# Optimization experiments

Measured on AMD Instinct MI355X. Metric: run time of the kernel, lower is better.

Reference implementation:

```python
import jax, jax.numpy as jnp
import numpy as np


def setup_inputs() -> dict:
    key = jax.random.key(0)
    ks = jax.random.split(key, 9)
    B, S, D, DK, DV = 4, 4096, 1024, 128, 128
    scale = 1.0 / np.sqrt(D)
    return {
        "q": jax.random.normal(ks[0], (B, S, D), jnp.float32),
        "k": jax.random.normal(ks[1], (B, S, D), jnp.float32),
        "v": jax.random.normal(ks[2], (B, S, D), jnp.float32),
        "Wq": jax.random.normal(ks[3], (D, DK), jnp.float32) * scale,
        "bq": jnp.zeros((DK,), jnp.float32),
        "Wk": jax.random.normal(ks[4], (D, DK), jnp.float32) * scale,
        "bk": jnp.zeros((DK,), jnp.float32),
        "Wv": jax.random.normal(ks[5], (D, DV), jnp.float32) * scale,
        "bv": jnp.zeros((DV,), jnp.float32),
    }


def reference(q, k, v, Wq, bq, Wk, bk, Wv, bv):
    # Q/K/V projections (nn.Linear)
    Q = q @ Wq + bq          # [B,S,DK]
    K = k @ Wk + bk          # [B,S,DK]
    V = v @ Wv + bv          # [B,S,DV]
    scale = Q.shape[-1] ** 0.5
    scores = jnp.einsum("bqd,bkd->bqk", Q, K) / scale  # [B,Sq,Sk]
    attn = jax.nn.softmax(scores, axis=-1)
    return jnp.einsum("bqk,bkd->bqd", attn, V)          # [B,Sq,DV]
```

## Files before the change

### kernel.cpp

```cpp
#include <hip/hip_runtime.h>
#include <hip/hip_bf16.h>
#include <cstdint>
#include <cmath>


typedef __bf16 bf16x8 __attribute__((ext_vector_type(8)));
typedef float f32x4 __attribute__((ext_vector_type(4)));
typedef float f32x16 __attribute__((ext_vector_type(16)));

__device__ __forceinline__ unsigned short f2bf(float f) {
  unsigned u = __float_as_uint(f);
  u += 0x7fffu + ((u >> 16) & 1u);
  return (unsigned short)(u >> 16);
}

__device__ __forceinline__ bf16x8 ld_frag(const char* p) {
  uint4 u = *reinterpret_cast<const uint4*>(p);
  return __builtin_bit_cast(bf16x8, u);
}

__device__ __forceinline__ unsigned cvtpk_bf16(float lo, float hi) {
  unsigned r;
  asm("v_cvt_pk_bf16_f32 %0, %1, %2" : "=v"(r) : "v"(lo), "v"(hi));
  return r;
}

__device__ __forceinline__ void pl32swap(unsigned &a, unsigned &b) {
  asm("v_permlane32_swap_b32 %0, %1" : "+v"(a), "+v"(b));
}

__device__ __forceinline__ bf16x8 mk_frag(unsigned w0, unsigned w1, unsigned w2, unsigned w3) {
  uint4 u{w0, w1, w2, w3};
  return __builtin_bit_cast(bf16x8, u);
}

#define QSCALE_LOG2E 0.12751744f

__global__ __launch_bounds__(256) void prep_wt_kernel(const float* __restrict__ W,
                                                      unsigned short* __restrict__ Wt) {
  __shared__ float tile[64][65];
  int kt = blockIdx.x, nt = blockIdx.y;
  int tid = threadIdx.x;
  int c = tid & 63;
  int r0 = (tid >> 6) * 16;
#pragma unroll
  for (int i = 0; i < 16; ++i) {
    int r = r0 + i;
    tile[r][c] = W[(size_t)(kt * 64 + r) * 128 + nt * 64 + c];
  }
  __syncthreads();
#pragma unroll
  for (int i = 0; i < 16; ++i) {
    int n = r0 + i;
    Wt[(size_t)(nt * 64 + n) * 1024 + kt * 64 + c] = f2bf(tile[c][n]);
  }
}

__global__ __launch_bounds__(256) void proj_kernel(
    const float* __restrict__ qx, const float* __restrict__ kx, const float* __restrict__ vx,
    const unsigned short* __restrict__ Wtq, const unsigned short* __restrict__ Wtk,
    const unsigned short* __restrict__ Wtv,
    const float* __restrict__ bq, const float* __restrict__ bk, const float* __restrict__ bv,
    unsigned short* __restrict__ Qb, unsigned short* __restrict__ Kb,
    unsigned short* __restrict__ Vtb) {
  const int mode = blockIdx.y;
  const float* x = (mode == 0) ? qx : (mode == 1) ? kx : vx;
  const unsigned short* Wt = (mode == 0) ? Wtq : (mode == 1) ? Wtk : Wtv;
  const float* bias = (mode == 0) ? bq : (mode == 1) ? bk : bv;

  __shared__ uint4 ldsA4[1024];
  __shared__ uint4 ldsW4[1024];
  char* ldsA = (char*)ldsA4;
  char* ldsW = (char*)ldsW4;

  const int tid = threadIdx.x;
  const int lane = tid & 63, wid = tid >> 6;
  const int l15 = lane & 15, hi = lane >> 4;
  const int wm = wid >> 1, wn = wid & 1;
  const long row0 = (long)blockIdx.x * 128;

  f32x4 acc[4][4];
#pragma unroll
  for (int i = 0; i < 4; ++i)
#pragma unroll
    for (int j = 0; j < 4; ++j) acc[i][j] = f32x4{0.f, 0.f, 0.f, 0.f};

  for (int kt = 0; kt < 16; ++kt) {
    const int k0 = kt * 64;
#pragma unroll
    for (int i = 0; i < 4; ++i) {
      int u = tid + 256 * i;
      int row = u >> 3, c8 = u & 7;
      const float* src = x + (row0 + row) * 1024 + k0 + c8 * 8;
      float4 f0 = *reinterpret_cast<const float4*>(src);
      float4 f1 = *reinterpret_cast<const float4*>(src + 4);
      uint4 w;
      w.x = (unsigned)f2bf(f0.x) | ((unsigned)f2bf(f0.y) << 16);
      w.y = (unsigned)f2bf(f0.z) | ((unsigned)f2bf(f0.w) << 16);
      w.z = (unsigned)f2bf(f1.x) | ((unsigned)f2bf(f1.y) << 16);
      w.w = (unsigned)f2bf(f1.z) | ((unsigned)f2bf(f1.w) << 16);
      int off = (row * 128 + c8 * 16) ^ ((row & 7) << 4);
      *reinterpret_cast<uint4*>(ldsA + off) = w;
      const unsigned short* wsrc = Wt + (size_t)row * 1024 + k0 + c8 * 8;
      uint4 wv = *reinterpret_cast<const uint4*>(wsrc);
      *reinterpret_cast<uint4*>(ldsW + off) = wv;
    }
    __syncthreads();
#pragma unroll
    for (int kk = 0; kk < 2; ++kk) {
      bf16x8 af[4], bfv[4];
#pragma unroll
      for (int mi = 0; mi < 4; ++mi) {
        int row = wm * 64 + mi * 16 + l15;
        af[mi] = ld_frag(ldsA + ((row * 128 + kk * 64 + hi * 16) ^ ((row & 7) << 4)));
      }
#pragma unroll
      for (int ni = 0; ni < 4; ++ni) {
        int row = wn * 64 + ni * 16 + l15;
        bfv[ni] = ld_frag(ldsW + ((row * 128 + kk * 64 + hi * 16) ^ ((row & 7) << 4)));
      }
#pragma unroll
      for (int mi = 0; mi < 4; ++mi)
#pragma unroll
        for (int ni = 0; ni < 4; ++ni)
          acc[mi][ni] = __builtin_amdgcn_mfma_f32_16x16x32_bf16(af[mi], bfv[ni], acc[mi][ni], 0, 0, 0);
    }
    __syncthreads();
  }

#pragma unroll
  for (int ni = 0; ni < 4; ++ni) {
    int n = wn * 64 + ni * 16 + l15;
    float bv_ = bias[n];
#pragma unroll
    for (int mi = 0; mi < 4; ++mi) {
      long m = row0 + wm * 64 + mi * 16 + hi * 4;
      f32x4 a = acc[mi][ni];
      if (mode == 2) {
        int bb = (int)(m >> 12);
        int s = (int)(m & 4095);
        ushort4 pk;
        pk.x = f2bf(a.x + bv_); pk.y = f2bf(a.y + bv_);
        pk.z = f2bf(a.z + bv_); pk.w = f2bf(a.w + bv_);
        *reinterpret_cast<ushort4*>(Vtb + ((size_t)(bb * 128 + n)) * 4096 + s) = pk;
      } else {
        const float sc = (mode == 0) ? QSCALE_LOG2E : 1.0f;
        unsigned short* outp = (mode == 0) ? Qb : Kb;
        outp[(m + 0) * 128 + n] = f2bf((a.x + bv_) * sc);
        outp[(m + 1) * 128 + n] = f2bf((a.y + bv_) * sc);
        outp[(m + 2) * 128 + n] = f2bf((a.z + bv_) * sc);
        outp[(m + 3) * 128 + n] = f2bf((a.w + bv_) * sc);
      }
    }
  }
}

__global__ __launch_bounds__(256, 2) void attn_kernel(
    const unsigned short* __restrict__ Qb, const unsigned short* __restrict__ Kb,
    const unsigned short* __restrict__ Vtb, float* __restrict__ Po,
    float* __restrict__ ml, int tps) {
  __shared__ uint4 ldsK4[1024];
  __shared__ uint4 ldsV4[1024];
  char* ldsK = (char*)ldsK4;
  char* ldsV = (char*)ldsV4;

  const int tid = threadIdx.x;
  const int lane = tid & 63, wid = tid >> 6;
  const int l31 = lane & 31, hi = lane >> 5;
  const int split = blockIdx.y;
  const int b = blockIdx.z;
  const int qbase = blockIdx.x * 128 + wid * 32;
  const size_t growq = (size_t)b * 4096 + qbase + l31;

  bf16x8 qf[8];
  {
    const unsigned short* qp = Qb + growq * 128 + hi * 8;
#pragma unroll
    for (int kt = 0; kt < 8; ++kt)
      qf[kt] = __builtin_bit_cast(bf16x8, *reinterpret_cast<const uint4*>(qp + kt * 16));
  }

  f32x16 oacc[4];
#pragma unroll
  for (int d = 0; d < 4; ++d)
#pragma unroll
    for (int j = 0; j < 16; ++j) oacc[d][j] = 0.f;
  float mrun = -INFINITY, lrun = 0.f;

  const int t0 = split * tps, t1 = t0 + tps;

  for (int t = t0; t < t1; ++t) {
    const int kv0 = t * 64;
    const char* kg = (const char*)Kb + ((size_t)(b * 4096) + kv0) * 256;
#pragma unroll
    for (int i = 0; i < 4; ++i) {
      int u = tid + 256 * i;
      int row = u >> 4, c = u & 15;
      uint4 val = *reinterpret_cast<const uint4*>(kg + row * 256 + c * 16);
      *reinterpret_cast<uint4*>(ldsK + ((row * 256 + c * 16) ^ ((row & 7) << 4))) = val;
    }
    const char* vg = (const char*)Vtb + (size_t)b * 128 * 4096 * 2 + (size_t)kv0 * 2;
#pragma unroll
    for (int i = 0; i < 4; ++i) {
      int u = tid + 256 * i;
      int dv = u >> 3, c = u & 7;
      uint4 val = *reinterpret_cast<const uint4*>(vg + (size_t)dv * 8192 + c * 16);
      *reinterpret_cast<uint4*>(ldsV + ((dv * 128 + c * 16) ^ ((dv & 7) << 4))) = val;
    }
    __syncthreads();

    f32x16 sc0, sc1;
#pragma unroll
    for (int j = 0; j < 16; ++j) { sc0[j] = 0.f; sc1[j] = 0.f; }
    __builtin_amdgcn_s_setprio(1);
#pragma unroll
    for (int kvb = 0; kvb < 2; ++kvb) {
      int row = kvb * 32 + l31;
      int rowoff = row * 256, swz = (row & 7) << 4;
#pragma unroll
      for (int kt = 0; kt < 8; ++kt) {
        bf16x8 kf = ld_frag(ldsK + ((rowoff + kt * 32 + hi * 16) ^ swz));
        if (kvb == 0) sc0 = __builtin_amdgcn_mfma_f32_32x32x16_bf16(kf, qf[kt], sc0, 0, 0, 0);
        else          sc1 = __builtin_amdgcn_mfma_f32_32x32x16_bf16(kf, qf[kt], sc1, 0, 0, 0);
      }
    }
    __builtin_amdgcn_s_setprio(0);

    float tmx[16];
#pragma unroll
    for (int i = 0; i < 16; ++i) tmx[i] = fmaxf(sc0[i], sc1[i]);
#pragma unroll
    for (int s = 8; s > 0; s >>= 1)
#pragma unroll
      for (int i = 0; i < s; ++i) tmx[i] = fmaxf(tmx[i], tmx[i + s]);
    float mt = tmx[0];
    mt = fmaxf(mt, __shfl_xor(mt, 32));

    if (!__all(mt - mrun <= 8.0f)) {
      float mnew = fmaxf(mrun, mt);
      float scl = exp2f(mrun - mnew);
      mrun = mnew;
      lrun *= scl;
#pragma unroll
      for (int d = 0; d < 4; ++d)
#pragma unroll
        for (int j = 0; j < 16; ++j) oacc[d][j] *= scl;
    }

#pragma unroll
    for (int i = 0; i < 16; ++i) {
      sc0[i] = exp2f(sc0[i] - mrun);
      sc1[i] = exp2f(sc1[i] - mrun);
    }
    float ts[16];
#pragma unroll
    for (int i = 0; i < 16; ++i) ts[i] = sc0[i] + sc1[i];
#pragma unroll
    for (int s = 8; s > 0; s >>= 1)
#pragma unroll
      for (int i = 0; i < s; ++i) ts[i] += ts[i + s];
    float psum = ts[0];
    psum += __shfl_xor(psum, 32);
    lrun += psum;

    bf16x8 pa[4];
#pragma unroll
    for (int c = 0; c < 2; ++c) {
      const f32x16& p = c ? sc1 : sc0;
#pragma unroll
      for (int g = 0; g < 2; ++g) {
        const int base = g * 8;
        unsigned a0 = cvtpk_bf16(p[base + 0], p[base + 1]);
        unsigned b0 = cvtpk_bf16(p[base + 4], p[base + 5]);
        pl32swap(a0, b0);
        unsigned a1 = cvtpk_bf16(p[base + 2], p[base + 3]);
        unsigned b1 = cvtpk_bf16(p[base + 6], p[base + 7]);
        pl32swap(a1, b1);
        pa[c * 2 + g] = mk_frag(a0, a1, b0, b1);
      }
    }

    __builtin_amdgcn_s_setprio(1);
#pragma unroll
    for (int dvb = 0; dvb < 4; ++dvb) {
      int vrow = dvb * 32 + l31;
      int voff = vrow * 128, vswz = (vrow & 7) << 4;
#pragma unroll
      for (int tt = 0; tt < 4; ++tt) {
        bf16x8 vf = ld_frag(ldsV + ((voff + tt * 32 + hi * 16) ^ vswz));
        oacc[dvb] = __builtin_amdgcn_mfma_f32_32x32x16_bf16(vf, pa[tt], oacc[dvb], 0, 0, 0);
      }
    }
    __builtin_amdgcn_s_setprio(0);
    __syncthreads();
  }

  if (hi == 0) {
    float* mlp = ml + (size_t)split * 32768 + growq * 2;
    mlp[0] = mrun; mlp[1] = lrun;
  }

  float* po = Po + ((size_t)split << 21) + ((size_t)b * 4096 + qbase) * 128;
  char* tbase = ldsK + wid * 4096;
  for (int dvb = 0; dvb < 4; ++dvb) {
#pragma unroll
    for (int g = 0; g < 4; ++g) {
      float4 w4{oacc[dvb][g * 4 + 0], oacc[dvb][g * 4 + 1],
                oacc[dvb][g * 4 + 2], oacc[dvb][g * 4 + 3]};
      int off = (l31 * 128 + g * 32 + hi * 16) ^ ((l31 & 7) << 4);
      *reinterpret_cast<float4*>(tbase + off) = w4;
    }
    asm volatile("s_waitcnt lgkmcnt(0)" ::: "memory");
    __builtin_amdgcn_sched_barrier(0);
#pragma unroll
    for (int qq = 0; qq < 4; ++qq) {
      int q = qq * 8 + (lane >> 3);
      int off = (q * 128 + (lane & 7) * 16) ^ ((q & 7) << 4);
      float4 r4 = *reinterpret_cast<const float4*>(tbase + off);
      *reinterpret_cast<float4*>(po + (size_t)q * 128 + dvb * 32 + (lane & 7) * 4) = r4;
    }
    asm volatile("s_waitcnt lgkmcnt(0)" ::: "memory");
    __builtin_amdgcn_sched_barrier(0);
  }
}

template <int NS>
__global__ __launch_bounds__(256) void combine_kernel(const float* __restrict__ Po,
                                                      const float* __restrict__ ml,
                                                      float* __restrict__ out) {
  int idx = blockIdx.x * 256 + threadIdx.x;
  int grow = idx >> 5;
  int c4 = (idx & 31) * 4;
  float m[NS], l[NS];
  float M = -INFINITY;
#pragma unroll
  for (int s = 0; s < NS; ++s) {
    m[s] = ml[(size_t)s * 32768 + grow * 2 + 0];
    l[s] = ml[(size_t)s * 32768 + grow * 2 + 1];
    M = fmaxf(M, m[s]);
  }
  float L = 0.f, w[NS];
#pragma unroll
  for (int s = 0; s < NS; ++s) {
    w[s] = exp2f(m[s] - M);
    L += l[s] * w[s];
  }
  float invL = 1.0f / L;
  float4 acc = {0.f, 0.f, 0.f, 0.f};
#pragma unroll
  for (int s = 0; s < NS; ++s) {
    float4 p = *reinterpret_cast<const float4*>(Po + ((size_t)s << 21) + (size_t)grow * 128 + c4);
    acc.x += p.x * w[s]; acc.y += p.y * w[s];
    acc.z += p.z * w[s]; acc.w += p.w * w[s];
  }
  acc.x *= invL; acc.y *= invL; acc.z *= invL; acc.w *= invL;
  *reinterpret_cast<float4*>(out + (size_t)grow * 128 + c4) = acc;
}

extern "C" void kernel_launch(void* const* d_in, const int* in_sizes, int n_in,
                              void* d_out, int out_size, void* d_ws, size_t ws_size,
                              hipStream_t stream) {
  const float* q  = (const float*)d_in[0];
  const float* k  = (const float*)d_in[1];
  const float* v  = (const float*)d_in[2];
  const float* Wq = (const float*)d_in[3];
  const float* bq = (const float*)d_in[4];
  const float* Wk = (const float*)d_in[5];
  const float* bk = (const float*)d_in[6];
  const float* Wv = (const float*)d_in[7];
  const float* bv = (const float*)d_in[8];
  float* out = (float*)d_out;

  char* ws = (char*)d_ws;
  unsigned short* Qb  = (unsigned short*)(ws);
  unsigned short* Kb  = (unsigned short*)(ws + (4u << 20));
  unsigned short* Vtb = (unsigned short*)(ws + (8u << 20));
  unsigned short* Wtq = (unsigned short*)(ws + (12u << 20));
  unsigned short* Wtk = (unsigned short*)(ws + (12u << 20) + (256u << 10));
  unsigned short* Wtv = (unsigned short*)(ws + (12u << 20) + (512u << 10));

  const size_t base = (size_t)13 << 20;
  const size_t per = ((size_t)8 << 20) + ((size_t)128 << 10);
  int nsplit = 1;
  if (ws_size >= base + 4 * per) nsplit = 4;
  else if (ws_size >= base + 2 * per) nsplit = 2;
  float* Po = (float*)(ws + base);
  float* ml = (float*)(ws + base + (size_t)nsplit * ((size_t)8 << 20));

  prep_wt_kernel<<<dim3(16, 2), 256, 0, stream>>>(Wq, Wtq);
  prep_wt_kernel<<<dim3(16, 2), 256, 0, stream>>>(Wk, Wtk);
  prep_wt_kernel<<<dim3(16, 2), 256, 0, stream>>>(Wv, Wtv);
  proj_kernel<<<dim3(128, 3), 256, 0, stream>>>(q, k, v, Wtq, Wtk, Wtv, bq, bk, bv, Qb, Kb, Vtb);
  attn_kernel<<<dim3(32, nsplit, 4), 256, 0, stream>>>(Qb, Kb, Vtb, Po, ml, 64 / nsplit);
  if (nsplit == 4)      combine_kernel<4><<<2048, 256, 0, stream>>>(Po, ml, out);
  else if (nsplit == 2) combine_kernel<2><<<2048, 256, 0, stream>>>(Po, ml, out);
  else                  combine_kernel<1><<<2048, 256, 0, stream>>>(Po, ml, out);
}
```

Measured before the change: 108.2 us.

## Double-buffer projection GEMM with register prefetch and smaller M tiles

The projection kernel now prefetches the next K-slice of activations and weights into registers while MFMAs run on the current LDS buffer, then writes to a second LDS buffer. This removes one barrier per iteration and hides global load latency. The M tile shrinks from 128 to 64 rows, doubling the grid to 768 blocks so more CUs are busy. The kernel also adds a launch-bounds occupancy hint, uses the hardware packed bf16 convert, and merges the three weight-prep launches into one, at the cost of more LDS per block and more weight reloads per output row.

Result: slower. 110.6 us (+2.2%).

```diff
diff --git a/kernel.cpp b/kernel.cpp
--- a/kernel.cpp
+++ b/kernel.cpp
@@ -36,8 +36,13 @@
 
 #define QSCALE_LOG2E 0.12751744f
 
-__global__ __launch_bounds__(256) void prep_wt_kernel(const float* __restrict__ W,
-                                                      unsigned short* __restrict__ Wt) {
+__global__ __launch_bounds__(256) void prep_wt_kernel(
+    const float* __restrict__ W0, const float* __restrict__ W1, const float* __restrict__ W2,
+    unsigned short* __restrict__ T0, unsigned short* __restrict__ T1,
+    unsigned short* __restrict__ T2) {
+  const int mode = blockIdx.z;
+  const float* W = (mode == 0) ? W0 : (mode == 1) ? W1 : W2;
+  unsigned short* Wt = (mode == 0) ? T0 : (mode == 1) ? T1 : T2;
   __shared__ float tile[64][65];
   int kt = blockIdx.x, nt = blockIdx.y;
   int tid = threadIdx.x;
@@ -56,7 +61,7 @@
   }
 }
 
-__global__ __launch_bounds__(256) void proj_kernel(
+__global__ __launch_bounds__(256, 4) void proj_kernel(
     const float* __restrict__ qx, const float* __restrict__ kx, const float* __restrict__ vx,
     const unsigned short* __restrict__ Wtq, const unsigned short* __restrict__ Wtk,
     const unsigned short* __restrict__ Wtv,
@@ -68,64 +73,95 @@
   const unsigned short* Wt = (mode == 0) ? Wtq : (mode == 1) ? Wtk : Wtv;
   const float* bias = (mode == 0) ? bq : (mode == 1) ? bk : bv;
 
-  __shared__ uint4 ldsA4[1024];
-  __shared__ uint4 ldsW4[1024];
-  char* ldsA = (char*)ldsA4;
-  char* ldsW = (char*)ldsW4;
+  __shared__ char lds[49152];
 
   const int tid = threadIdx.x;
   const int lane = tid & 63, wid = tid >> 6;
   const int l15 = lane & 15, hi = lane >> 4;
   const int wm = wid >> 1, wn = wid & 1;
-  const long row0 = (long)blockIdx.x * 128;
-
-  f32x4 acc[4][4];
-#pragma unroll
-  for (int i = 0; i < 4; ++i)
+  const long row0 = (long)blockIdx.x * 64;
+
+  const int arow = tid >> 2, ac16 = tid & 3;
+  const int wrow = tid >> 1, wc32 = tid & 1;
+  const int aswz = (arow & 7) << 4;
+  const int aoff0 = (arow * 128 + ac16 * 32) ^ aswz;
+  const int aoff1 = (arow * 128 + ac16 * 32 + 16) ^ aswz;
+  const int wswz = (wrow & 7) << 4;
+  int woff[4];
+#pragma unroll
+  for (int i = 0; i < 4; ++i) woff[i] = (wrow * 128 + wc32 * 64 + i * 16) ^ wswz;
+
+  const float* asrc0 = x + (row0 + arow) * 1024 + ac16 * 16;
+  const unsigned short* wsrc0 = Wt + (size_t)wrow * 1024 + wc32 * 32;
+
+  f32x4 acc[2][4];
+#pragma unroll
+  for (int i = 0; i < 2; ++i)
 #pragma unroll
     for (int j = 0; j < 4; ++j) acc[i][j] = f32x4{0.f, 0.f, 0.f, 0.f};
 
+  float4 apf[4];
+  uint4 wpf[4];
+#pragma unroll
+  for (int i = 0; i < 4; ++i) apf[i] = *reinterpret_cast<const float4*>(asrc0 + i * 4);
+#pragma unroll
+  for (int i = 0; i < 4; ++i) wpf[i] = *reinterpret_cast<const uint4*>(wsrc0 + i * 8);
+  {
+    uint4 p0{cvtpk_bf16(apf[0].x, apf[0].y), cvtpk_bf16(apf[0].z, apf[0].w),
+             cvtpk_bf16(apf[1].x, apf[1].y), cvtpk_bf16(apf[1].z, apf[1].w)};
+    uint4 p1{cvtpk_bf16(apf[2].x, apf[2].y), cvtpk_bf16(apf[2].z, apf[2].w),
+             cvtpk_bf16(apf[3].x, apf[3].y), cvtpk_bf16(apf[3].z, apf[3].w)};
+    *reinterpret_cast<uint4*>(lds + aoff0) = p0;
+    *reinterpret_cast<uint4*>(lds + aoff1) = p1;
+#pragma unroll
+    for (int i = 0; i < 4; ++i) *reinterpret_cast<uint4*>(lds + 16384 + woff[i]) = wpf[i];
+  }
+  __syncthreads();
+
+  int cur = 0;
   for (int kt = 0; kt < 16; ++kt) {
-    const int k0 = kt * 64;
-#pragma unroll
-    for (int i = 0; i < 4; ++i) {
-      int u = tid + 256 * i;
-      int row = u >> 3, c8 = u & 7;
-      const float* src = x + (row0 + row) * 1024 + k0 + c8 * 8;
-      float4 f0 = *reinterpret_cast<const float4*>(src);
-      float4 f1 = *reinterpret_cast<const float4*>(src + 4);
-      uint4 w;
-      w.x = (unsigned)f2bf(f0.x) | ((unsigned)f2bf(f0.y) << 16);
-      w.y = (unsigned)f2bf(f0.z) | ((unsigned)f2bf(f0.w) << 16);
-      w.z = (unsigned)f2bf(f1.x) | ((unsigned)f2bf(f1.y) << 16);
-      w.w = (unsigned)f2bf(f1.z) | ((unsigned)f2bf(f1.w) << 16);
-      int off = (row * 128 + c8 * 16) ^ ((row & 7) << 4);
-      *reinterpret_cast<uint4*>(ldsA + off) = w;
-      const unsigned short* wsrc = Wt + (size_t)row * 1024 + k0 + c8 * 8;
-      uint4 wv = *reinterpret_cast<const uint4*>(wsrc);
-      *reinterpret_cast<uint4*>(ldsW + off) = wv;
-    }
-    __syncthreads();
+    if (kt < 15) {
+      const int k1 = (kt + 1) * 64;
+#pragma unroll
+      for (int i = 0; i < 4; ++i) apf[i] = *reinterpret_cast<const float4*>(asrc0 + k1 + i * 4);
+#pragma unroll
+      for (int i = 0; i < 4; ++i) wpf[i] = *reinterpret_cast<const uint4*>(wsrc0 + k1 + i * 8);
+    }
+    char* bufA = lds + cur * 8192;
+    char* bufW = lds + 16384 + cur * 16384;
 #pragma unroll
     for (int kk = 0; kk < 2; ++kk) {
-      bf16x8 af[4], bfv[4];
-#pragma unroll
-      for (int mi = 0; mi < 4; ++mi) {
-        int row = wm * 64 + mi * 16 + l15;
-        af[mi] = ld_frag(ldsA + ((row * 128 + kk * 64 + hi * 16) ^ ((row & 7) << 4)));
+      bf16x8 af[2], wf[4];
+#pragma unroll
+      for (int mi = 0; mi < 2; ++mi) {
+        int row = wm * 32 + mi * 16 + l15;
+        af[mi] = ld_frag(bufA + ((row * 128 + kk * 64 + hi * 16) ^ ((row & 7) << 4)));
       }
 #pragma unroll
       for (int ni = 0; ni < 4; ++ni) {
         int row = wn * 64 + ni * 16 + l15;
-        bfv[ni] = ld_frag(ldsW + ((row * 128 + kk * 64 + hi * 16) ^ ((row & 7) << 4)));
-      }
-#pragma unroll
-      for (int mi = 0; mi < 4; ++mi)
+        wf[ni] = ld_frag(bufW + ((row * 128 + kk * 64 + hi * 16) ^ ((row & 7) << 4)));
+      }
+#pragma unroll
+      for (int mi = 0; mi < 2; ++mi)
 #pragma unroll
         for (int ni = 0; ni < 4; ++ni)
-          acc[mi][ni] = __builtin_amdgcn_mfma_f32_16x16x32_bf16(af[mi], bfv[ni], acc[mi][ni], 0, 0, 0);
-    }
-    __syncthreads();
+          acc[mi][ni] = __builtin_amdgcn_mfma_f32_16x16x32_bf16(af[mi], wf[ni], acc[mi][ni], 0, 0, 0);
+    }
+    if (kt < 15) {
+      char* nA = lds + (cur ^ 1) * 8192;
+      char* nW = lds + 16384 + (cur ^ 1) * 16384;
+      uint4 p0{cvtpk_bf16(apf[0].x, apf[0].y), cvtpk_bf16(apf[0].z, apf[0].w),
+               cvtpk_bf16(apf[1].x, apf[1].y), cvtpk_bf16(apf[1].z, apf[1].w)};
+      uint4 p1{cvtpk_bf16(apf[2].x, apf[2].y), cvtpk_bf16(apf[2].z, apf[2].w),
+               cvtpk_bf16(apf[3].x, apf[3].y), cvtpk_bf16(apf[3].z, apf[3].w)};
+      *reinterpret_cast<uint4*>(nA + aoff0) = p0;
+      *reinterpret_cast<uint4*>(nA + aoff1) = p1;
+#pragma unroll
+      for (int i = 0; i < 4; ++i) *reinterpret_cast<uint4*>(nW + woff[i]) = wpf[i];
+      __syncthreads();
+      cur ^= 1;
+    }
   }
 
 #pragma unroll
@@ -133,8 +169,8 @@
     int n = wn * 64 + ni * 16 + l15;
     float bv_ = bias[n];
 #pragma unroll
-    for (int mi = 0; mi < 4; ++mi) {
-      long m = row0 + wm * 64 + mi * 16 + hi * 4;
+    for (int mi = 0; mi < 2; ++mi) {
+      long m = row0 + wm * 32 + mi * 16 + hi * 4;
       f32x4 a = acc[mi][ni];
       if (mode == 2) {
         int bb = (int)(m >> 12);
@@ -387,10 +423,8 @@
   float* Po = (float*)(ws + base);
   float* ml = (float*)(ws + base + (size_t)nsplit * ((size_t)8 << 20));
 
-  prep_wt_kernel<<<dim3(16, 2), 256, 0, stream>>>(Wq, Wtq);
-  prep_wt_kernel<<<dim3(16, 2), 256, 0, stream>>>(Wk, Wtk);
-  prep_wt_kernel<<<dim3(16, 2), 256, 0, stream>>>(Wv, Wtv);
-  proj_kernel<<<dim3(128, 3), 256, 0, stream>>>(q, k, v, Wtq, Wtk, Wtv, bq, bk, bv, Qb, Kb, Vtb);
+  prep_wt_kernel<<<dim3(16, 2, 3), 256, 0, stream>>>(Wq, Wk, Wv, Wtq, Wtk, Wtv);
+  proj_kernel<<<dim3(256, 3), 256, 0, stream>>>(q, k, v, Wtq, Wtk, Wtv, bq, bk, bv, Qb, Kb, Vtb);
   attn_kernel<<<dim3(32, nsplit, 4), 256, 0, stream>>>(Qb, Kb, Vtb, Po, ml, 64 / nsplit);
   if (nsplit == 4)      combine_kernel<4><<<2048, 256, 0, stream>>>(Po, ml, out);
   else if (nsplit == 2) combine_kernel<2><<<2048, 256, 0, stream>>>(Po, ml, out);
```

## Rewrite projection GEMM to load operands straight into registers, merge weight-prep launches

Applied to the files above, without the earlier changes.

The projection kernel drops its LDS staging and barriers. Each wave now owns 16 rows and all 128 output columns, loading fp32 activations directly into registers with a one-step prefetch, converting them with packed bf16 conversion, and reading weight fragments straight from global memory. The grid doubles to 768 blocks with a higher occupancy hint. The three weight-transpose launches are merged into one 3D launch. The risk is that weights are re-read from global/L2 by every wave with no LDS reuse, and the direct A loads are less coalesced.

Result: slower. 175.7 us (+62.4%).

```diff
diff --git a/kernel.cpp b/kernel.cpp
--- a/kernel.cpp
+++ b/kernel.cpp
@@ -34,10 +34,20 @@
   return __builtin_bit_cast(bf16x8, u);
 }
 
+__device__ __forceinline__ bf16x8 cvt_frag(const float4& f0, const float4& f1) {
+  return mk_frag(cvtpk_bf16(f0.x, f0.y), cvtpk_bf16(f0.z, f0.w),
+                 cvtpk_bf16(f1.x, f1.y), cvtpk_bf16(f1.z, f1.w));
+}
+
 #define QSCALE_LOG2E 0.12751744f
 
-__global__ __launch_bounds__(256) void prep_wt_kernel(const float* __restrict__ W,
-                                                      unsigned short* __restrict__ Wt) {
+__global__ __launch_bounds__(256) void prep_wt_kernel(
+    const float* __restrict__ W0, const float* __restrict__ W1, const float* __restrict__ W2,
+    unsigned short* __restrict__ T0, unsigned short* __restrict__ T1,
+    unsigned short* __restrict__ T2) {
+  const int mode = blockIdx.z;
+  const float* W = (mode == 0) ? W0 : (mode == 1) ? W1 : W2;
+  unsigned short* Wt = (mode == 0) ? T0 : (mode == 1) ? T1 : T2;
   __shared__ float tile[64][65];
   int kt = blockIdx.x, nt = blockIdx.y;
   int tid = threadIdx.x;
@@ -56,7 +66,7 @@
   }
 }
 
-__global__ __launch_bounds__(256) void proj_kernel(
+__global__ __launch_bounds__(256, 4) void proj_kernel(
     const float* __restrict__ qx, const float* __restrict__ kx, const float* __restrict__ vx,
     const unsigned short* __restrict__ Wtq, const unsigned short* __restrict__ Wtk,
     const unsigned short* __restrict__ Wtv,
@@ -68,89 +78,64 @@
   const unsigned short* Wt = (mode == 0) ? Wtq : (mode == 1) ? Wtk : Wtv;
   const float* bias = (mode == 0) ? bq : (mode == 1) ? bk : bv;
 
-  __shared__ uint4 ldsA4[1024];
-  __shared__ uint4 ldsW4[1024];
-  char* ldsA = (char*)ldsA4;
-  char* ldsW = (char*)ldsW4;
-
   const int tid = threadIdx.x;
   const int lane = tid & 63, wid = tid >> 6;
   const int l15 = lane & 15, hi = lane >> 4;
-  const int wm = wid >> 1, wn = wid & 1;
-  const long row0 = (long)blockIdx.x * 128;
-
-  f32x4 acc[4][4];
-#pragma unroll
-  for (int i = 0; i < 4; ++i)
-#pragma unroll
-    for (int j = 0; j < 4; ++j) acc[i][j] = f32x4{0.f, 0.f, 0.f, 0.f};
-
-  for (int kt = 0; kt < 16; ++kt) {
-    const int k0 = kt * 64;
-#pragma unroll
-    for (int i = 0; i < 4; ++i) {
-      int u = tid + 256 * i;
-      int row = u >> 3, c8 = u & 7;
-      const float* src = x + (row0 + row) * 1024 + k0 + c8 * 8;
-      float4 f0 = *reinterpret_cast<const float4*>(src);
-      float4 f1 = *reinterpret_cast<const float4*>(src + 4);
-      uint4 w;
-      w.x = (unsigned)f2bf(f0.x) | ((unsigned)f2bf(f0.y) << 16);
-      w.y = (unsigned)f2bf(f0.z) | ((unsigned)f2bf(f0.w) << 16);
-      w.z = (unsigned)f2bf(f1.x) | ((unsigned)f2bf(f1.y) << 16);
-      w.w = (unsigned)f2bf(f1.z) | ((unsigned)f2bf(f1.w) << 16);
-      int off = (row * 128 + c8 * 16) ^ ((row & 7) << 4);
-      *reinterpret_cast<uint4*>(ldsA + off) = w;
-      const unsigned short* wsrc = Wt + (size_t)row * 1024 + k0 + c8 * 8;
-      uint4 wv = *reinterpret_cast<const uint4*>(wsrc);
-      *reinterpret_cast<uint4*>(ldsW + off) = wv;
-    }
-    __syncthreads();
-#pragma unroll
-    for (int kk = 0; kk < 2; ++kk) {
-      bf16x8 af[4], bfv[4];
-#pragma unroll
-      for (int mi = 0; mi < 4; ++mi) {
-        int row = wm * 64 + mi * 16 + l15;
-        af[mi] = ld_frag(ldsA + ((row * 128 + kk * 64 + hi * 16) ^ ((row & 7) << 4)));
-      }
-#pragma unroll
-      for (int ni = 0; ni < 4; ++ni) {
-        int row = wn * 64 + ni * 16 + l15;
-        bfv[ni] = ld_frag(ldsW + ((row * 128 + kk * 64 + hi * 16) ^ ((row & 7) << 4)));
-      }
-#pragma unroll
-      for (int mi = 0; mi < 4; ++mi)
-#pragma unroll
-        for (int ni = 0; ni < 4; ++ni)
-          acc[mi][ni] = __builtin_amdgcn_mfma_f32_16x16x32_bf16(af[mi], bfv[ni], acc[mi][ni], 0, 0, 0);
-    }
-    __syncthreads();
-  }
-
-#pragma unroll
-  for (int ni = 0; ni < 4; ++ni) {
-    int n = wn * 64 + ni * 16 + l15;
+  const long m0 = (long)blockIdx.x * 64 + wid * 16;
+
+  const float* abase = x + (m0 + l15) * 1024 + hi * 8;
+  const char* wbase = (const char*)Wt + (size_t)l15 * 2048 + hi * 16;
+
+  f32x4 acc[8];
+#pragma unroll
+  for (int i = 0; i < 8; ++i) acc[i] = f32x4{0.f, 0.f, 0.f, 0.f};
+
+  float4 a00 = *reinterpret_cast<const float4*>(abase + 0);
+  float4 a01 = *reinterpret_cast<const float4*>(abase + 4);
+  float4 a10 = *reinterpret_cast<const float4*>(abase + 32);
+  float4 a11 = *reinterpret_cast<const float4*>(abase + 36);
+
+#pragma unroll 1
+  for (int t = 0; t < 16; ++t) {
+    bf16x8 af0 = cvt_frag(a00, a01);
+    bf16x8 af1 = cvt_frag(a10, a11);
+    if (t < 15) {
+      const float* an = abase + (t + 1) * 64;
+      a00 = *reinterpret_cast<const float4*>(an + 0);
+      a01 = *reinterpret_cast<const float4*>(an + 4);
+      a10 = *reinterpret_cast<const float4*>(an + 32);
+      a11 = *reinterpret_cast<const float4*>(an + 36);
+    }
+    const char* wt_ = wbase + t * 128;
+#pragma unroll
+    for (int ni = 0; ni < 8; ++ni) {
+      bf16x8 wf0 = ld_frag(wt_ + (size_t)ni * 32768);
+      bf16x8 wf1 = ld_frag(wt_ + (size_t)ni * 32768 + 64);
+      acc[ni] = __builtin_amdgcn_mfma_f32_16x16x32_bf16(af0, wf0, acc[ni], 0, 0, 0);
+      acc[ni] = __builtin_amdgcn_mfma_f32_16x16x32_bf16(af1, wf1, acc[ni], 0, 0, 0);
+    }
+  }
+
+#pragma unroll
+  for (int ni = 0; ni < 8; ++ni) {
+    int n = ni * 16 + l15;
     float bv_ = bias[n];
-#pragma unroll
-    for (int mi = 0; mi < 4; ++mi) {
-      long m = row0 + wm * 64 + mi * 16 + hi * 4;
-      f32x4 a = acc[mi][ni];
-      if (mode == 2) {
-        int bb = (int)(m >> 12);
-        int s = (int)(m & 4095);
-        ushort4 pk;
-        pk.x = f2bf(a.x + bv_); pk.y = f2bf(a.y + bv_);
-        pk.z = f2bf(a.z + bv_); pk.w = f2bf(a.w + bv_);
-        *reinterpret_cast<ushort4*>(Vtb + ((size_t)(bb * 128 + n)) * 4096 + s) = pk;
-      } else {
-        const float sc = (mode == 0) ? QSCALE_LOG2E : 1.0f;
-        unsigned short* outp = (mode == 0) ? Qb : Kb;
-        outp[(m + 0) * 128 + n] = f2bf((a.x + bv_) * sc);
-        outp[(m + 1) * 128 + n] = f2bf((a.y + bv_) * sc);
-        outp[(m + 2) * 128 + n] = f2bf((a.z + bv_) * sc);
-        outp[(m + 3) * 128 + n] = f2bf((a.w + bv_) * sc);
-      }
+    long m = m0 + hi * 4;
+    f32x4 a = acc[ni];
+    if (mode == 2) {
+      int bb = (int)(m >> 12);
+      int s = (int)(m & 4095);
+      ushort4 pk;
+      pk.x = f2bf(a.x + bv_); pk.y = f2bf(a.y + bv_);
+      pk.z = f2bf(a.z + bv_); pk.w = f2bf(a.w + bv_);
+      *reinterpret_cast<ushort4*>(Vtb + ((size_t)(bb * 128 + n)) * 4096 + s) = pk;
+    } else {
+      const float sc = (mode == 0) ? QSCALE_LOG2E : 1.0f;
+      unsigned short* outp = (mode == 0) ? Qb : Kb;
+      outp[(m + 0) * 128 + n] = f2bf((a.x + bv_) * sc);
+      outp[(m + 1) * 128 + n] = f2bf((a.y + bv_) * sc);
+      outp[(m + 2) * 128 + n] = f2bf((a.z + bv_) * sc);
+      outp[(m + 3) * 128 + n] = f2bf((a.w + bv_) * sc);
     }
   }
 }
@@ -387,10 +372,8 @@
   float* Po = (float*)(ws + base);
   float* ml = (float*)(ws + base + (size_t)nsplit * ((size_t)8 << 20));
 
-  prep_wt_kernel<<<dim3(16, 2), 256, 0, stream>>>(Wq, Wtq);
-  prep_wt_kernel<<<dim3(16, 2), 256, 0, stream>>>(Wk, Wtk);
-  prep_wt_kernel<<<dim3(16, 2), 256, 0, stream>>>(Wv, Wtv);
-  proj_kernel<<<dim3(128, 3), 256, 0, stream>>>(q, k, v, Wtq, Wtk, Wtv, bq, bk, bv, Qb, Kb, Vtb);
+  prep_wt_kernel<<<dim3(16, 2, 3), 256, 0, stream>>>(Wq, Wk, Wv, Wtq, Wtk, Wtv);
+  proj_kernel<<<dim3(256, 3), 256, 0, stream>>>(q, k, v, Wtq, Wtk, Wtv, bq, bk, bv, Qb, Kb, Vtb);
   attn_kernel<<<dim3(32, nsplit, 4), 256, 0, stream>>>(Qb, Kb, Vtb, Po, ml, 64 / nsplit);
   if (nsplit == 4)      combine_kernel<4><<<2048, 256, 0, stream>>>(Po, ml, out);
   else if (nsplit == 2) combine_kernel<2><<<2048, 256, 0, stream>>>(Po, ml, out);
```
